# Optimization experiments

Measured on AMD Instinct MI355X. Metric: run time of the kernel, lower is better.

Reference implementation:

```python
import jax, jax.numpy as jnp
import numpy as np


def setup_inputs() -> dict:
    key = jax.random.key(0)
    x = jax.random.normal(key, (32, 1, 1024, 1024), dtype=jnp.float32)
    return {"x": x}


def reference(x) -> jnp.ndarray:
    # Original torch loop computes a running max down the height dim (dim=2)
    # for channel 0 (C=1 here), overwriting each element with the prefix max.
    # This is exactly a cumulative-max (prefix-max scan) along axis=2.
    return jax.lax.associative_scan(jnp.maximum, x, axis=2)
```

## Files before the change

kernel.cpp:

```cpp
#include <hip/hip_runtime.h>


constexpr int B = 32;
constexpr int H = 1024;
constexpr int W = 1024;
constexpr int ROW4 = W / 4;
constexpr int SW4 = 8;
constexpr int NSTRIP = ROW4 / SW4;
constexpr int CH = 128;
constexpr int NCHUNK = H / CH;
constexpr int R = 4;

__device__ __forceinline__ float4 max4(float4 a, float4 b) {
    return make_float4(fmaxf(a.x, b.x), fmaxf(a.y, b.y),
                       fmaxf(a.z, b.z), fmaxf(a.w, b.w));
}

__device__ __forceinline__ float4 shflup4(float4 v, int d) {
    float4 r;
    r.x = __shfl_up(v.x, d, 64);
    r.y = __shfl_up(v.y, d, 64);
    r.z = __shfl_up(v.z, d, 64);
    r.w = __shfl_up(v.w, d, 64);
    return r;
}

__global__ __launch_bounds__(256) void cummax_sp(const float* __restrict__ xf,
                                                 float* __restrict__ of) {
    __shared__ float4 wavetot[2][32];

    const int tid = threadIdx.x;
    const int lane = tid & 63;
    const int wid = tid >> 6;
    const int w = tid & 7;
    const int hsegG = tid >> 3;
    const int hseg_l = (tid >> 3) & 7;

    const int b = blockIdx.x >> 5;
    const int strip = blockIdx.x & (NSTRIP - 1);
    const float4* x4 = (const float4*)xf;
    float4* o4 = (float4*)of;
    const size_t tbase = (size_t)b * (H * ROW4) + (size_t)strip * SW4 + w;

    const float ninf = -__builtin_inff();
    const float4 ninf4 = make_float4(ninf, ninf, ninf, ninf);
    float4 carry = ninf4;

    float4 cur[R], nxt[R];

#pragma unroll
    for (int r = 0; r < R; ++r)
        cur[r] = x4[tbase + (size_t)(hsegG * R + r) * ROW4];

#pragma unroll
    for (int c = 0; c < NCHUNK; ++c) {
        if (c + 1 < NCHUNK) {
#pragma unroll
            for (int r = 0; r < R; ++r)
                nxt[r] = x4[tbase + (size_t)((c + 1) * CH + hsegG * R + r) * ROW4];
        }

        float4 m = max4(max4(cur[0], cur[1]), max4(cur[2], cur[3]));

        float4 incl = m;
        { float4 t = shflup4(incl, 8);  if (lane >= 8)  incl = max4(incl, t); }
        { float4 t = shflup4(incl, 16); if (lane >= 16) incl = max4(incl, t); }
        { float4 t = shflup4(incl, 32); if (lane >= 32) incl = max4(incl, t); }
        float4 ew = shflup4(incl, 8);
        float4 excl = (hseg_l == 0) ? ninf4 : ew;

        if (hseg_l == 7) wavetot[c & 1][wid * 8 + w] = incl;
        __syncthreads();

        float4 crosspre = carry;
        float4 tot = carry;
#pragma unroll
        for (int w2 = 0; w2 < 4; ++w2) {
            float4 v = wavetot[c & 1][w2 * 8 + w];
            if (w2 < wid) crosspre = max4(crosspre, v);
            tot = max4(tot, v);
        }
        carry = tot;

        float4 a = max4(crosspre, excl);
#pragma unroll
        for (int r = 0; r < R; ++r) {
            a = max4(a, cur[r]);
            o4[tbase + (size_t)(c * CH + hsegG * R + r) * ROW4] = a;
        }

        if (c + 1 < NCHUNK) {
#pragma unroll
            for (int r = 0; r < R; ++r) cur[r] = nxt[r];
        }
    }
}

extern "C" void kernel_launch(void* const* d_in, const int* in_sizes, int n_in,
                              void* d_out, int out_size, void* d_ws, size_t ws_size,
                              hipStream_t stream) {
    const float* x = (const float*)d_in[0];
    float* out = (float*)d_out;
    cummax_sp<<<B * NSTRIP, 256, 0, stream>>>(x, out);
}
```

Measured before the change: 240.6 us.

## Widen strips to 16 float4 columns, use 512-thread blocks and two-chunk prefetch

Result: no change. 240.8 us (+0.1%).

```diff
diff --git a/kernel.cpp b/kernel.cpp
--- a/kernel.cpp
+++ b/kernel.cpp
@@ -5,11 +5,14 @@
 constexpr int H = 1024;
 constexpr int W = 1024;
 constexpr int ROW4 = W / 4;
-constexpr int SW4 = 8;
+constexpr int SW4 = 16;
 constexpr int NSTRIP = ROW4 / SW4;
-constexpr int CH = 128;
+constexpr int NT = 512;
+constexpr int NWAVE = NT / 64;
+constexpr int NSEG = NT / SW4;
+constexpr int R = 4;
+constexpr int CH = NSEG * R;
 constexpr int NCHUNK = H / CH;
-constexpr int R = 4;
 
 __device__ __forceinline__ float4 max4(float4 a, float4 b) {
     return make_float4(fmaxf(a.x, b.x), fmaxf(a.y, b.y),
@@ -25,18 +28,18 @@
     return r;
 }
 
-__global__ __launch_bounds__(256) void cummax_sp(const float* __restrict__ xf,
-                                                 float* __restrict__ of) {
-    __shared__ float4 wavetot[2][32];
+__global__ __launch_bounds__(512, 4) void cummax_sp2(const float* __restrict__ xf,
+                                                     float* __restrict__ of) {
+    __shared__ float4 wavetot[2][NWAVE][SW4];
 
     const int tid = threadIdx.x;
     const int lane = tid & 63;
     const int wid = tid >> 6;
-    const int w = tid & 7;
-    const int hsegG = tid >> 3;
-    const int hseg_l = (tid >> 3) & 7;
+    const int w = tid & (SW4 - 1);
+    const int hsegG = tid >> 4;
+    const int hseg_l = (tid >> 4) & 3;
 
-    const int b = blockIdx.x >> 5;
+    const int b = blockIdx.x >> 4;
     const int strip = blockIdx.x & (NSTRIP - 1);
     const float4* x4 = (const float4*)xf;
     float4* o4 = (float4*)of;
@@ -46,37 +49,36 @@
     const float4 ninf4 = make_float4(ninf, ninf, ninf, ninf);
     float4 carry = ninf4;
 
-    float4 cur[R], nxt[R];
+    float4 c0[R], c1[R], c2[R];
 
-#pragma unroll
-    for (int r = 0; r < R; ++r)
-        cur[r] = x4[tbase + (size_t)(hsegG * R + r) * ROW4];
+#define LDCHUNK(c, dst)                                                      \
+    _Pragma("unroll")                                                        \
+    for (int r = 0; r < R; ++r)                                              \
+        dst[r] = x4[tbase + (size_t)((c) * CH + hsegG * R + r) * ROW4];
+
+    LDCHUNK(0, c0);
+    LDCHUNK(1, c1);
 
 #pragma unroll
     for (int c = 0; c < NCHUNK; ++c) {
-        if (c + 1 < NCHUNK) {
-#pragma unroll
-            for (int r = 0; r < R; ++r)
-                nxt[r] = x4[tbase + (size_t)((c + 1) * CH + hsegG * R + r) * ROW4];
-        }
+        if (c + 2 < NCHUNK) { LDCHUNK(c + 2, c2); }
 
-        float4 m = max4(max4(cur[0], cur[1]), max4(cur[2], cur[3]));
+        float4 m = max4(max4(c0[0], c0[1]), max4(c0[2], c0[3]));
 
         float4 incl = m;
-        { float4 t = shflup4(incl, 8);  if (lane >= 8)  incl = max4(incl, t); }
         { float4 t = shflup4(incl, 16); if (lane >= 16) incl = max4(incl, t); }
         { float4 t = shflup4(incl, 32); if (lane >= 32) incl = max4(incl, t); }
-        float4 ew = shflup4(incl, 8);
+        float4 ew = shflup4(incl, 16);
         float4 excl = (hseg_l == 0) ? ninf4 : ew;
 
-        if (hseg_l == 7) wavetot[c & 1][wid * 8 + w] = incl;
+        if (hseg_l == 3) wavetot[c & 1][wid][w] = incl;
         __syncthreads();
 
         float4 crosspre = carry;
         float4 tot = carry;
 #pragma unroll
-        for (int w2 = 0; w2 < 4; ++w2) {
-            float4 v = wavetot[c & 1][w2 * 8 + w];
+        for (int w2 = 0; w2 < NWAVE; ++w2) {
+            float4 v = wavetot[c & 1][w2][w];
             if (w2 < wid) crosspre = max4(crosspre, v);
             tot = max4(tot, v);
         }
@@ -85,15 +87,14 @@
         float4 a = max4(crosspre, excl);
 #pragma unroll
         for (int r = 0; r < R; ++r) {
-            a = max4(a, cur[r]);
+            a = max4(a, c0[r]);
             o4[tbase + (size_t)(c * CH + hsegG * R + r) * ROW4] = a;
         }
 
-        if (c + 1 < NCHUNK) {
 #pragma unroll
-            for (int r = 0; r < R; ++r) cur[r] = nxt[r];
-        }
+        for (int r = 0; r < R; ++r) { c0[r] = c1[r]; c1[r] = c2[r]; }
     }
+#undef LDCHUNK
 }
 
 extern "C" void kernel_launch(void* const* d_in, const int* in_sizes, int n_in,
@@ -101,5 +102,5 @@
                               hipStream_t stream) {
     const float* x = (const float*)d_in[0];
     float* out = (float*)d_out;
-    cummax_sp<<<B * NSTRIP, 256, 0, stream>>>(x, out);
+    cummax_sp2<<<B * NSTRIP, NT, 0, stream>>>(x, out);
 }
```
